# Kernel optimization log

Measured on AMD Instinct MI355X. Metric: run time of the kernel, lower is better.

The kernel has to match this reference:

```python
import jax, jax.numpy as jnp
import numpy as np

H = 768          # hidden_size
V = 32000        # vocab_size
NUM_GATES = 5    # none/dontcare/ptr/yes/no
PAD = 0          # pad_token_id


def setup_inputs() -> dict:
    key = jax.random.key(0)
    ks = jax.random.split(key, 10)
    B, S, J, Ls = 16, 512, 30, 4
    max_len = 8
    sc = 1.0 / np.sqrt(H).astype(np.float32)
    E = jax.random.normal(ks[0], (V, H), jnp.float32) * sc
    E = E.at[PAD].set(0.0)  # padding_idx row is zero
    return dict(
        input_ids=jax.random.randint(ks[1], (B, S), 0, V),
        encoder_output=jax.random.normal(ks[2], (B, S, H), jnp.float32),
        hidden=jax.random.normal(ks[3], (1, B, H), jnp.float32),
        input_masks=jnp.ones((B, S), jnp.int32),  # 1 = valid token
        slot=jax.random.randint(ks[4], (J, Ls), 0, V),
        max_len=max_len,
        E=E,
        W_ih=jax.random.normal(ks[5], (3 * H, H), jnp.float32) * sc,
        W_hh=jax.random.normal(ks[6], (3 * H, H), jnp.float32) * sc,
        b_ih=jnp.zeros((3 * H,), jnp.float32),
        b_hh=jnp.zeros((3 * H,), jnp.float32),
        W_gen=jax.random.normal(ks[7], (3 * H, 1), jnp.float32) * sc,
        b_gen=jnp.zeros((1,), jnp.float32),
        W_gate=jax.random.normal(ks[8], (H, NUM_GATES), jnp.float32) * sc,
        b_gate=jnp.zeros((NUM_GATES,), jnp.float32),
    )


def gru_step(x, h, W_ih, W_hh, b_ih, b_hh):
    # PyTorch GRUCell math
    gi = x @ W_ih.T + b_ih
    gh = h @ W_hh.T + b_hh
    ir, iz, inn = jnp.split(gi, 3, axis=-1)
    hr, hz, hn = jnp.split(gh, 3, axis=-1)
    r = jax.nn.sigmoid(ir + hr)
    z = jax.nn.sigmoid(iz + hz)
    n = jnp.tanh(inn + r * hn)
    return (1.0 - z) * n + z * h


def reference(input_ids, encoder_output, hidden, input_masks, slot, max_len,
              E, W_ih, W_hh, b_ih, b_hh, W_gen, b_gen, W_gate, b_gate):
    B, S, Hd = encoder_output.shape
    J = slot.shape[0]
    mask = input_masks != 1                         # True -> masked (pad)
    slot_e = E[slot].sum(axis=1)                    # [J, H]
    BJ = B * J
    # parallel decoding: flat index = b*J + j (matches repeat/repeat_interleave)
    w = jnp.tile(slot_e, (B, 1))                    # [BJ, H]
    h = jnp.repeat(hidden[0], J, axis=0)            # [BJ, H]
    enc = jnp.repeat(encoder_output, J, axis=0)     # [BJ, S, H]
    ids = jnp.repeat(input_ids, J, axis=0)          # [BJ, S]
    msk = jnp.repeat(mask, J, axis=0)               # [BJ, S]
    rows = jnp.arange(BJ)

    def step(carry, _):
        w, h = carry
        h = gru_step(w, h, W_ih, W_hh, b_ih, b_hh)                    # [BJ, H]
        attn_e = jnp.einsum('bsh,bh->bs', enc, h)                     # [BJ, S]
        attn_e = jnp.where(msk, -1e9, attn_e)
        attn_history = jax.nn.softmax(attn_e, axis=-1)                # [BJ, S]
        attn_vocab = jax.nn.softmax(h @ E.T, axis=-1)                 # [BJ, V]
        context = jnp.einsum('bs,bsh->bh', attn_history, enc)         # [BJ, H]
        p_gen = jax.nn.sigmoid(
            jnp.concatenate([w, h, context], -1) @ W_gen + b_gen)     # [BJ, 1]
        ptr = jnp.zeros_like(attn_vocab).at[rows[:, None], ids].add(attn_history)
        p_final = p_gen * attn_vocab + (1.0 - p_gen) * ptr            # [BJ, V]
        w_next = E[jnp.argmax(p_final, axis=-1)]                      # greedy (teacher=None)
        return (w_next, h), (p_final, context)

    (_, _), (points, contexts) = jax.lax.scan(step, (w, h), None, length=max_len)
    gate_logit = contexts[0] @ W_gate + b_gate                        # gate from step k==0
    all_points = points.transpose(1, 0, 2).reshape(B, J, max_len, V)
    all_gates = gate_logit.reshape(B, J, NUM_GATES)
    return all_points, all_gates
```

## Files before the change

### kernel.cpp

```cpp
#include <hip/hip_runtime.h>
#include <cstdint>
#include <cstddef>

#define HDIM 768
#define VOCAB 32000
#define NGATES 5
#define NJ 30
#define NB 16
#define NS 512
#define NBJ (NB*NJ)
#define G3 2304
#define PR 608
#define NBV 250

typedef _Float16 f16;
typedef _Float16 f16x8 __attribute__((ext_vector_type(8)));
typedef float f32x4 __attribute__((ext_vector_type(4)));

#define GLOBAL_AS __attribute__((address_space(1)))
#define LDS_AS    __attribute__((address_space(3)))

__global__ void k_cast(const float* __restrict__ src, f16* __restrict__ dst, int n) {
    for (int i = blockIdx.x*256 + threadIdx.x; i < n; i += gridDim.x*256)
        dst[i] = (f16)src[i];
}

__global__ void k_cast_split(const float* __restrict__ src, f16* __restrict__ hi,
                             f16* __restrict__ lo, int n) {
    for (int i = blockIdx.x*256 + threadIdx.x; i < n; i += gridDim.x*256) {
        float v = src[i];
        f16 h = (f16)v;
        hi[i] = h;
        lo[i] = (f16)(v - (float)h);
    }
}

__global__ void k_tsplit(const float* __restrict__ enc,
                         f16* __restrict__ encH, f16* __restrict__ encL,
                         f16* __restrict__ encTH, f16* __restrict__ encTL) {
    __shared__ float tile[32][33];
    const int b = blockIdx.x, s0 = blockIdx.y*32, h0 = blockIdx.z*32;
    const int t = threadIdx.x;
    const int hl = t & 31, sl = t >> 5;
    #pragma unroll
    for (int r = 0; r < 4; ++r) {
        int ss = sl + r*8;
        float v = enc[((long)b*NS + s0 + ss)*HDIM + h0 + hl];
        tile[ss][hl] = v;
        f16 h = (f16)v;
        long o = ((long)b*NS + s0 + ss)*HDIM + h0 + hl;
        encH[o] = h; encL[o] = (f16)(v - (float)h);
    }
    __syncthreads();
    #pragma unroll
    for (int r = 0; r < 4; ++r) {
        int hh = sl + r*8;
        float v = tile[hl][hh];
        f16 h = (f16)v;
        long o = ((long)b*HDIM + h0 + hh)*NS + s0 + hl;
        encTH[o] = h; encTL[o] = (f16)(v - (float)h);
    }
}

__global__ void k_init_state(const float* __restrict__ E, const int* __restrict__ slot,
                             const float* __restrict__ hidden,
                             f16* __restrict__ w_hi, f16* __restrict__ w_lo,
                             float* __restrict__ h,
                             f16* __restrict__ h_hi, f16* __restrict__ h_lo) {
    int total = NBJ*HDIM;
    for (int i = blockIdx.x*256 + threadIdx.x; i < total; i += gridDim.x*256) {
        int hh = i % HDIM, row = i / HDIM;
        int b = row / NJ, j = row % NJ;
        float s = 0.f;
        #pragma unroll
        for (int l = 0; l < 4; ++l) s += E[(long)slot[j*4+l]*HDIM + hh];
        f16 sh = (f16)s;
        w_hi[i] = sh; w_lo[i] = (f16)(s - (float)sh);
        float hv = hidden[b*HDIM + hh];
        h[i] = hv;
        f16 hh16 = (f16)hv;
        h_hi[i] = hh16; h_lo[i] = (f16)(hv - (float)hh16);
    }
}

__launch_bounds__(256)
__global__ void k_gemm(const f16* __restrict__ Ah, const f16* __restrict__ Al,
                       const f16* __restrict__ Bh, const f16* __restrict__ Bl,
                       float* __restrict__ Cp, float* __restrict__ psum,
                       int M, long ldc, long coff, int kdim, int nspan,
                       long aBS, long bBS, long cBS) {
    __shared__ f16 a_lds[8][128][8];
    __shared__ f16 b_lds[8][128][8];
    __shared__ float sbuf[2][128];

    const int tid = threadIdx.x;
    const int z = blockIdx.z;
    const int m0 = blockIdx.x*128, n0 = blockIdx.y*128;
    const int w = tid >> 6, lane = tid & 63;
    const int wm = (w >> 1)*64, wn = (w & 1)*64;
    const int lr = lane & 15, lg = lane >> 4;

    f32x4 acc[4][4] = {};

    for (int sp = 0; sp < nspan; ++sp) {
        const f16* Ap = ((sp < 2) ? Ah : Al) + (long)z*aBS;
        const f16* Bp = ((sp == 1) ? Bl : Bh) + (long)z*bBS;
        for (int kc = 0; kc < kdim; kc += 64) {
            #pragma unroll
            for (int i = 0; i < 4; ++i) {
                const int idx = w*4 + i;
                const int c = idx >> 1;
                const int rl = (idx & 1)*64 + lane;
                const f16* ga = Ap + (long)(m0 + rl)*kdim + kc + c*8;
                const f16* gb = Bp + (long)(n0 + rl)*kdim + kc + c*8;
                __builtin_amdgcn_global_load_lds(
                    (const GLOBAL_AS unsigned int*)ga,
                    (LDS_AS unsigned int*)((char*)&a_lds[0][0][0] + idx*1024), 16, 0, 0);
                __builtin_amdgcn_global_load_lds(
                    (const GLOBAL_AS unsigned int*)gb,
                    (LDS_AS unsigned int*)((char*)&b_lds[0][0][0] + idx*1024), 16, 0, 0);
            }
            __syncthreads();
            #pragma unroll
            for (int kk = 0; kk < 2; ++kk) {
                const int c = kk*4 + lg;
                f16x8 af[4], bf[4];
                #pragma unroll
                for (int mi = 0; mi < 4; ++mi) af[mi] = *(const f16x8*)&a_lds[c][wm + mi*16 + lr][0];
                #pragma unroll
                for (int nf = 0; nf < 4; ++nf) bf[nf] = *(const f16x8*)&b_lds[c][wn + nf*16 + lr][0];
                #pragma unroll
                for (int mi = 0; mi < 4; ++mi)
                    #pragma unroll
                    for (int nf = 0; nf < 4; ++nf)
                        acc[mi][nf] = __builtin_amdgcn_mfma_f32_16x16x32_f16(af[mi], bf[nf], acc[mi][nf], 0, 0, 0);
            }
            __syncthreads();
        }
    }

    float* Cb = Cp + (long)z*cBS + coff;
    #pragma unroll
    for (int mi = 0; mi < 4; ++mi) {
        #pragma unroll
        for (int nf = 0; nf < 4; ++nf) {
            int col = n0 + wn + nf*16 + lr;
            int rowb = m0 + wm + mi*16 + lg*4;
            #pragma unroll
            for (int r = 0; r < 4; ++r) {
                int row = rowb + r;
                if (row < M) Cb[(long)row*ldc + col] = acc[mi][nf][r];
            }
        }
    }

    if (psum != nullptr) {
        #pragma unroll
        for (int mi = 0; mi < 4; ++mi) {
            #pragma unroll
            for (int r = 0; r < 4; ++r) {
                float s = 0.f;
                #pragma unroll
                for (int nf = 0; nf < 4; ++nf) s += expf(acc[mi][nf][r]);
                s += __shfl_xor(s, 1); s += __shfl_xor(s, 2);
                s += __shfl_xor(s, 4); s += __shfl_xor(s, 8);
                if (lr == 0) sbuf[w & 1][wm + mi*16 + lg*4 + r] = s;
            }
        }
        __syncthreads();
        if (tid < 128)
            psum[(long)blockIdx.y*512 + m0 + tid] = sbuf[0][tid] + sbuf[1][tid];
    }
}

__global__ void k_gru_elem(const float* __restrict__ gi, const float* __restrict__ gh,
                           const float* __restrict__ bih, const float* __restrict__ bhh,
                           float* __restrict__ h, f16* __restrict__ h_hi, f16* __restrict__ h_lo) {
    int total = NBJ*HDIM;
    for (int i = blockIdx.x*256 + threadIdx.x; i < total; i += gridDim.x*256) {
        int c = i % HDIM; long row = i / HDIM;
        long base = row*G3;
        float r = gi[base + c]        + bih[c]        + gh[base + c]        + bhh[c];
        float z = gi[base + 768 + c]  + bih[768 + c]  + gh[base + 768 + c]  + bhh[768 + c];
        float hn = gh[base + 1536 + c] + bhh[1536 + c];
        float in_ = gi[base + 1536 + c] + bih[1536 + c];
        r = 1.f/(1.f + expf(-r));
        z = 1.f/(1.f + expf(-z));
        float n = tanhf(in_ + r*hn);
        float hv = (1.f - z)*n + z*h[i];
        h[i] = hv;
        f16 hh16 = (f16)hv;
        h_hi[i] = hh16; h_lo[i] = (f16)(hv - (float)hh16);
    }
}

__launch_bounds__(256)
__global__ void k_softmax_s(float* __restrict__ ae, const int* __restrict__ masks,
                            f16* __restrict__ ahH, f16* __restrict__ ahL) {
    const int row = blockIdx.x, tid = threadIdx.x;
    const int b = row / NJ;
    __shared__ float red[256];
    float x0 = ae[(long)row*NS + tid];
    float x1 = ae[(long)row*NS + tid + 256];
    if (masks[b*NS + tid]       != 1) x0 = -1e9f;
    if (masks[b*NS + tid + 256] != 1) x1 = -1e9f;
    red[tid] = fmaxf(x0, x1); __syncthreads();
    for (int o = 128; o > 0; o >>= 1) { if (tid < o) red[tid] = fmaxf(red[tid], red[tid+o]); __syncthreads(); }
    float m = red[0]; __syncthreads();
    float e0 = expf(x0 - m), e1 = expf(x1 - m);
    red[tid] = e0 + e1; __syncthreads();
    for (int o = 128; o > 0; o >>= 1) { if (tid < o) red[tid] += red[tid+o]; __syncthreads(); }
    float inv = 1.f/red[0];
    float p0 = e0*inv, p1 = e1*inv;
    ae[(long)row*NS + tid]       = p0;
    ae[(long)row*NS + tid + 256] = p1;
    f16 a0 = (f16)p0, a1 = (f16)p1;
    ahH[(long)row*NS + tid]       = a0; ahL[(long)row*NS + tid]       = (f16)(p0 - (float)a0);
    ahH[(long)row*NS + tid + 256] = a1; ahL[(long)row*NS + tid + 256] = (f16)(p1 - (float)a1);
}

__launch_bounds__(64)
__global__ void k_pgen(const f16* __restrict__ w_hi, const f16* __restrict__ w_lo,
                       const float* __restrict__ h,
                       const float* __restrict__ ctx, const float* __restrict__ Wgen,
                       const float* __restrict__ bgen, const float* __restrict__ Wgate,
                       const float* __restrict__ bgate, float* __restrict__ pgen,
                       float* __restrict__ out_gates, int do_gate) {
    const int row = blockIdx.x, lane = threadIdx.x;
    float acc = 0.f;
    for (int x = lane; x < HDIM; x += 64) {
        float wv = (float)w_hi[(long)row*HDIM + x] + (float)w_lo[(long)row*HDIM + x];
        acc += wv                          * Wgen[x];
        acc += h[(long)row*HDIM + x]       * Wgen[768 + x];
        acc += ctx[(long)row*HDIM + x]     * Wgen[1536 + x];
    }
    for (int o = 32; o > 0; o >>= 1) acc += __shfl_down(acc, o);
    if (lane == 0) pgen[row] = 1.f/(1.f + expf(-(acc + bgen[0])));
    if (do_gate) {
        for (int g = 0; g < NGATES; ++g) {
            float a = 0.f;
            for (int x = lane; x < HDIM; x += 64) a += ctx[(long)row*HDIM + x]*Wgate[x*NGATES + g];
            for (int o = 32; o > 0; o >>= 1) a += __shfl_down(a, o);
            if (lane == 0) out_gates[row*NGATES + g] = a + bgate[g];
        }
    }
}

__launch_bounds__(256)
__global__ void k_finalize(float* __restrict__ pts, long ldrow, long coff,
                           const float* __restrict__ psum, const float* __restrict__ pgen,
                           const int* __restrict__ ids, const float* __restrict__ ah,
                           const float* __restrict__ E,
                           f16* __restrict__ w_hi, f16* __restrict__ w_lo) {
    const int row = blockIdx.x, tid = threadIdx.x;
    const int b = row / NJ;
    float* base = pts + (long)row*ldrow + coff;

    __shared__ float red[256];
    float s = 0.f;
    for (int nb = tid; nb < NBV; nb += 256) s += psum[(long)nb*512 + row];
    red[tid] = s; __syncthreads();
    for (int o = 128; o > 0; o >>= 1) { if (tid < o) red[tid] += red[tid+o]; __syncthreads(); }
    const float pg = pgen[row];
    const float scale = pg / red[0];

    float bv = -1.f; int bi = 0;
    for (int v = tid; v < VOCAB; v += 256) {
        float val = scale*expf(base[v]);
        base[v] = val;
        if (val > bv) { bv = val; bi = v; }
    }
    __shared__ float rv[256]; __shared__ int ri[256];
    rv[tid] = bv; ri[tid] = bi; __syncthreads();
    for (int o = 128; o > 0; o >>= 1) {
        if (tid < o) {
            float v2 = rv[tid+o]; int i2 = ri[tid+o];
            if (v2 > rv[tid] || (v2 == rv[tid] && i2 < ri[tid])) { rv[tid] = v2; ri[tid] = i2; }
        }
        __syncthreads();
    }
    float v0 = rv[0]; int i0 = ri[0];
    __syncthreads();

    const float cp = 1.f - pg;
    float sv = -1.f; int si = 0x7FFFFFFF;
    for (int ss = tid; ss < NS; ss += 256) {
        int id = ids[(long)b*NS + ss];
        float add = cp * ah[(long)row*NS + ss];
        float old = atomicAdd(base + id, add);
        float cand = old + add;
        if (cand > sv || (cand == sv && id < si)) { sv = cand; si = id; }
    }
    rv[tid] = sv; ri[tid] = si; __syncthreads();
    for (int o = 128; o > 0; o >>= 1) {
        if (tid < o) {
            float v2 = rv[tid+o]; int i2 = ri[tid+o];
            if (v2 > rv[tid] || (v2 == rv[tid] && i2 < ri[tid])) { rv[tid] = v2; ri[tid] = i2; }
        }
        __syncthreads();
    }
    __shared__ int bidx;
    if (tid == 0) {
        int ii = i0; float vv = v0;
        if (rv[0] > vv || (rv[0] == vv && ri[0] < ii)) { vv = rv[0]; ii = ri[0]; }
        bidx = ii;
    }
    __syncthreads();
    const int idx = bidx;
    for (int x = tid; x < HDIM; x += 256) {
        float ev = E[(long)idx*HDIM + x];
        f16 eh = (f16)ev;
        w_hi[(long)row*HDIM + x] = eh;
        w_lo[(long)row*HDIM + x] = (f16)(ev - (float)eh);
    }
}

extern "C" void kernel_launch(void* const* d_in, const int* in_sizes, int n_in,
                              void* d_out, int out_size, void* d_ws, size_t ws_size,
                              hipStream_t stream) {
    const int*   input_ids = (const int*)  d_in[0];
    const float* enc       = (const float*)d_in[1];
    const float* hidden    = (const float*)d_in[2];
    const int*   masks     = (const int*)  d_in[3];
    const int*   slot      = (const int*)  d_in[4];
    const float* E     = (const float*)d_in[6];
    const float* Wih   = (const float*)d_in[7];
    const float* Whh   = (const float*)d_in[8];
    const float* bih   = (const float*)d_in[9];
    const float* bhh   = (const float*)d_in[10];
    const float* Wgen  = (const float*)d_in[11];
    const float* bgen  = (const float*)d_in[12];
    const float* Wgate = (const float*)d_in[13];
    const float* bgate = (const float*)d_in[14];

    const int ml = (out_size / NBJ - NGATES) / VOCAB;
    float* out = (float*)d_out;
    float* gates_out = out + (long)NBJ*ml*VOCAB;

    char* ws = (char*)d_ws;
    auto carve = [&](size_t bytes) { char* p = ws; ws += (bytes + 255) & ~(size_t)255; return p; };
    f16*   E16   = (f16*)carve((size_t)VOCAB*HDIM*2);
    f16*   WH2   = (f16*)carve((size_t)2*G3*HDIM*2);
    f16*   WL2   = (f16*)carve((size_t)2*G3*HDIM*2);
    f16*   SH    = (f16*)carve((size_t)2*PR*HDIM*2);
    f16*   SL    = (f16*)carve((size_t)2*PR*HDIM*2);
    float* gigh  = (float*)carve((size_t)2*NBJ*G3*4);
    f16*   encH  = (f16*)carve((size_t)NB*NS*HDIM*2);
    f16*   encL  = (f16*)carve((size_t)NB*NS*HDIM*2);
    f16*   encTH = (f16*)carve((size_t)NB*HDIM*NS*2);
    f16*   encTL = (f16*)carve((size_t)NB*HDIM*NS*2);
    float* hbuf  = (float*)carve((size_t)NBJ*HDIM*4);
    float* ae    = (float*)carve((size_t)NBJ*NS*4);
    f16*   ahH   = (f16*)carve((size_t)PR*NS*2);
    f16*   ahL   = (f16*)carve((size_t)PR*NS*2);
    float* ctx   = (float*)carve((size_t)NBJ*HDIM*4);
    float* pgen  = (float*)carve((size_t)NBJ*4);
    float* ps    = (float*)carve((size_t)NBV*512*4);

    f16* WihH = WH2;  f16* WihL = WL2;
    f16* wH = SH;     f16* wL = SL;
    f16* hH = SH + (size_t)PR*HDIM;
    f16* hL = SL + (size_t)PR*HDIM;
    float* gi = gigh; float* gh = gigh + (size_t)NBJ*G3;

    k_cast<<<8192, 256, 0, stream>>>(E, E16, VOCAB*HDIM);
    k_cast_split<<<2048, 256, 0, stream>>>(Wih, WihH, WihL, G3*HDIM);
    k_cast_split<<<2048, 256, 0, stream>>>(Whh, WH2 + (size_t)G3*HDIM, WL2 + (size_t)G3*HDIM, G3*HDIM);
    k_tsplit<<<dim3(NB, 16, 24), 256, 0, stream>>>(enc, encH, encL, encTH, encTL);
    k_init_state<<<1440, 256, 0, stream>>>(E, slot, hidden, wH, wL, hbuf, hH, hL);

    const long ldrow = (long)ml*VOCAB;
    for (int t = 0; t < ml; ++t) {
        k_gemm<<<dim3(4, 18, 2), 256, 0, stream>>>(wH, wL, WihH, WihL, gigh, nullptr,
            NBJ, (long)G3, 0, HDIM, 3, (long)PR*HDIM, (long)G3*HDIM, (long)NBJ*G3);
        k_gru_elem<<<1440, 256, 0, stream>>>(gi, gh, bih, bhh, hbuf, hH, hL);
        k_gemm<<<dim3(1, 4, NB), 256, 0, stream>>>(hH, hL, encH, encL, ae, nullptr,
            NJ, (long)NS, 0, HDIM, 3, (long)NJ*HDIM, (long)NS*HDIM, (long)NJ*NS);
        k_softmax_s<<<NBJ, 256, 0, stream>>>(ae, masks, ahH, ahL);
        k_gemm<<<dim3(1, 6, NB), 256, 0, stream>>>(ahH, ahL, encTH, encTL, ctx, nullptr,
            NJ, (long)HDIM, 0, NS, 3, (long)NJ*NS, (long)HDIM*NS, (long)NJ*HDIM);
        k_pgen<<<NBJ, 64, 0, stream>>>(wH, wL, hbuf, ctx, Wgen, bgen, Wgate, bgate,
                                       pgen, gates_out, t == 0 ? 1 : 0);
        k_gemm<<<dim3(4, NBV, 1), 256, 0, stream>>>(hH, hL, E16, nullptr, out, ps,
            NBJ, ldrow, (long)t*VOCAB, HDIM, 1, 0, 0, 0);
        k_finalize<<<NBJ, 256, 0, stream>>>(out, ldrow, (long)t*VOCAB, ps, pgen,
                                            input_ids, ae, E, wH, wL);
    }
}
```

Measured before the change: 2.768 ms.

## Replace split-fp16 attention GEMMs with fp32 kernels and split vocab finalize

```diff
diff --git a/kernel.cpp b/kernel.cpp
--- a/kernel.cpp
+++ b/kernel.cpp
@@ -35,33 +35,6 @@
     }
 }
 
-__global__ void k_tsplit(const float* __restrict__ enc,
-                         f16* __restrict__ encH, f16* __restrict__ encL,
-                         f16* __restrict__ encTH, f16* __restrict__ encTL) {
-    __shared__ float tile[32][33];
-    const int b = blockIdx.x, s0 = blockIdx.y*32, h0 = blockIdx.z*32;
-    const int t = threadIdx.x;
-    const int hl = t & 31, sl = t >> 5;
-    #pragma unroll
-    for (int r = 0; r < 4; ++r) {
-        int ss = sl + r*8;
-        float v = enc[((long)b*NS + s0 + ss)*HDIM + h0 + hl];
-        tile[ss][hl] = v;
-        f16 h = (f16)v;
-        long o = ((long)b*NS + s0 + ss)*HDIM + h0 + hl;
-        encH[o] = h; encL[o] = (f16)(v - (float)h);
-    }
-    __syncthreads();
-    #pragma unroll
-    for (int r = 0; r < 4; ++r) {
-        int hh = sl + r*8;
-        float v = tile[hl][hh];
-        f16 h = (f16)v;
-        long o = ((long)b*HDIM + h0 + hh)*NS + s0 + hl;
-        encTH[o] = h; encTL[o] = (f16)(v - (float)h);
-    }
-}
-
 __global__ void k_init_state(const float* __restrict__ E, const int* __restrict__ slot,
                              const float* __restrict__ hidden,
                              f16* __restrict__ w_hi, f16* __restrict__ w_lo,
@@ -86,7 +59,8 @@
 __launch_bounds__(256)
 __global__ void k_gemm(const f16* __restrict__ Ah, const f16* __restrict__ Al,
                        const f16* __restrict__ Bh, const f16* __restrict__ Bl,
-                       float* __restrict__ Cp, float* __restrict__ psum,
+                       float* __restrict__ Cf, f16* __restrict__ Ch,
+                       float* __restrict__ psum,
                        int M, long ldc, long coff, int kdim, int nspan,
                        long aBS, long bBS, long cBS) {
     __shared__ f16 a_lds[8][128][8];
@@ -139,19 +113,34 @@
         }
     }
 
-    float* Cb = Cp + (long)z*cBS + coff;
-    #pragma unroll
-    for (int mi = 0; mi < 4; ++mi) {
-        #pragma unroll
-        for (int nf = 0; nf < 4; ++nf) {
-            int col = n0 + wn + nf*16 + lr;
-            int rowb = m0 + wm + mi*16 + lg*4;
-            #pragma unroll
-            for (int r = 0; r < 4; ++r) {
-                int row = rowb + r;
-                if (row < M) Cb[(long)row*ldc + col] = acc[mi][nf][r];
-            }
-        }
+    if (Ch != nullptr) {
+        f16* Cb = Ch + (long)z*cBS + coff;
+        #pragma unroll
+        for (int mi = 0; mi < 4; ++mi)
+            #pragma unroll
+            for (int nf = 0; nf < 4; ++nf) {
+                int col = n0 + wn + nf*16 + lr;
+                int rowb = m0 + wm + mi*16 + lg*4;
+                #pragma unroll
+                for (int r = 0; r < 4; ++r) {
+                    int row = rowb + r;
+                    if (row < M) Cb[(long)row*ldc + col] = (f16)acc[mi][nf][r];
+                }
+            }
+    } else {
+        float* Cb = Cf + (long)z*cBS + coff;
+        #pragma unroll
+        for (int mi = 0; mi < 4; ++mi)
+            #pragma unroll
+            for (int nf = 0; nf < 4; ++nf) {
+                int col = n0 + wn + nf*16 + lr;
+                int rowb = m0 + wm + mi*16 + lg*4;
+                #pragma unroll
+                for (int r = 0; r < 4; ++r) {
+                    int row = rowb + r;
+                    if (row < M) Cb[(long)row*ldc + col] = acc[mi][nf][r];
+                }
+            }
     }
 
     if (psum != nullptr) {
@@ -161,7 +150,7 @@
             for (int r = 0; r < 4; ++r) {
                 float s = 0.f;
                 #pragma unroll
-                for (int nf = 0; nf < 4; ++nf) s += expf(acc[mi][nf][r]);
+                for (int nf = 0; nf < 4; ++nf) s += expf((float)(f16)acc[mi][nf][r]);
                 s += __shfl_xor(s, 1); s += __shfl_xor(s, 2);
                 s += __shfl_xor(s, 4); s += __shfl_xor(s, 8);
                 if (lr == 0) sbuf[w & 1][wm + mi*16 + lg*4 + r] = s;
@@ -195,11 +184,60 @@
 }
 
 __launch_bounds__(256)
-__global__ void k_softmax_s(float* __restrict__ ae, const int* __restrict__ masks,
-                            f16* __restrict__ ahH, f16* __restrict__ ahL) {
+__global__ void k_attn(const float* __restrict__ h, const float* __restrict__ enc,
+                       float* __restrict__ attn_e) {
+    __shared__ float h_lds[NJ][64];
+    __shared__ float e_lds[64][65];
+    const int b = blockIdx.x, st = blockIdx.y;
+    const int s0 = st*64;
+    const int tid = threadIdx.x;
+    const int s = tid & 63, jg = tid >> 6;
+    float acc[8] = {};
+    for (int kc = 0; kc < HDIM; kc += 64) {
+        for (int idx = tid; idx < NJ*64; idx += 256) {
+            int j = idx >> 6, k = idx & 63;
+            h_lds[j][k] = h[((long)(b*NJ + j))*HDIM + kc + k];
+        }
+        #pragma unroll
+        for (int i = 0; i < 4; ++i) {
+            int id = tid + i*256;
+            int ss = id >> 4, kq = (id & 15)*4;
+            float4 v = *(const float4*)&enc[((long)b*NS + s0 + ss)*HDIM + kc + kq];
+            e_lds[ss][kq+0] = v.x; e_lds[ss][kq+1] = v.y;
+            e_lds[ss][kq+2] = v.z; e_lds[ss][kq+3] = v.w;
+        }
+        __syncthreads();
+        for (int k = 0; k < 64; ++k) {
+            float e = e_lds[s][k];
+            #pragma unroll
+            for (int i = 0; i < 8; ++i) {
+                int j = jg + i*4;
+                if (j < NJ) acc[i] += h_lds[j][k]*e;
+            }
+        }
+        __syncthreads();
+    }
+    #pragma unroll
+    for (int i = 0; i < 8; ++i) {
+        int j = jg + i*4;
+        if (j < NJ) attn_e[((long)(b*NJ + j))*NS + s0 + s] = acc[i];
+    }
+}
+
+__launch_bounds__(256)
+__global__ void k_smctxpg(float* __restrict__ ae, const int* __restrict__ masks,
+                          const float* __restrict__ enc,
+                          const f16* __restrict__ w_hi, const f16* __restrict__ w_lo,
+                          const float* __restrict__ h,
+                          const float* __restrict__ Wgen, const float* __restrict__ bgen,
+                          const float* __restrict__ Wgate, const float* __restrict__ bgate,
+                          float* __restrict__ pgen, float* __restrict__ out_gates, int do_gate) {
     const int row = blockIdx.x, tid = threadIdx.x;
     const int b = row / NJ;
     __shared__ float red[256];
+    __shared__ float ah_l[NS];
+    __shared__ float ctx_l[HDIM];
+
     float x0 = ae[(long)row*NS + tid];
     float x1 = ae[(long)row*NS + tid + 256];
     if (masks[b*NS + tid]       != 1) x0 = -1e9f;
@@ -214,60 +252,60 @@
     float p0 = e0*inv, p1 = e1*inv;
     ae[(long)row*NS + tid]       = p0;
     ae[(long)row*NS + tid + 256] = p1;
-    f16 a0 = (f16)p0, a1 = (f16)p1;
-    ahH[(long)row*NS + tid]       = a0; ahL[(long)row*NS + tid]       = (f16)(p0 - (float)a0);
-    ahH[(long)row*NS + tid + 256] = a1; ahL[(long)row*NS + tid + 256] = (f16)(p1 - (float)a1);
-}
-
-__launch_bounds__(64)
-__global__ void k_pgen(const f16* __restrict__ w_hi, const f16* __restrict__ w_lo,
-                       const float* __restrict__ h,
-                       const float* __restrict__ ctx, const float* __restrict__ Wgen,
-                       const float* __restrict__ bgen, const float* __restrict__ Wgate,
-                       const float* __restrict__ bgate, float* __restrict__ pgen,
-                       float* __restrict__ out_gates, int do_gate) {
-    const int row = blockIdx.x, lane = threadIdx.x;
+    ah_l[tid] = p0; ah_l[tid + 256] = p1;
+    __syncthreads();
+
+    const float* eb = enc + (long)b*NS*HDIM;
+    float c0 = 0.f, c1 = 0.f, c2 = 0.f;
+    for (int s = 0; s < NS; ++s) {
+        float a = ah_l[s];
+        const float* er = eb + (long)s*HDIM;
+        c0 += a*er[tid]; c1 += a*er[tid + 256]; c2 += a*er[tid + 512];
+    }
+    ctx_l[tid] = c0; ctx_l[tid + 256] = c1; ctx_l[tid + 512] = c2;
+    __syncthreads();
+
     float acc = 0.f;
-    for (int x = lane; x < HDIM; x += 64) {
+    for (int x = tid; x < HDIM; x += 256) {
         float wv = (float)w_hi[(long)row*HDIM + x] + (float)w_lo[(long)row*HDIM + x];
-        acc += wv                          * Wgen[x];
-        acc += h[(long)row*HDIM + x]       * Wgen[768 + x];
-        acc += ctx[(long)row*HDIM + x]     * Wgen[1536 + x];
-    }
-    for (int o = 32; o > 0; o >>= 1) acc += __shfl_down(acc, o);
-    if (lane == 0) pgen[row] = 1.f/(1.f + expf(-(acc + bgen[0])));
+        acc += wv*Wgen[x] + h[(long)row*HDIM + x]*Wgen[768 + x] + ctx_l[x]*Wgen[1536 + x];
+    }
+    red[tid] = acc; __syncthreads();
+    for (int o = 128; o > 0; o >>= 1) { if (tid < o) red[tid] += red[tid+o]; __syncthreads(); }
+    if (tid == 0) pgen[row] = 1.f/(1.f + expf(-(red[0] + bgen[0])));
+
     if (do_gate) {
         for (int g = 0; g < NGATES; ++g) {
+            __syncthreads();
             float a = 0.f;
-            for (int x = lane; x < HDIM; x += 64) a += ctx[(long)row*HDIM + x]*Wgate[x*NGATES + g];
-            for (int o = 32; o > 0; o >>= 1) a += __shfl_down(a, o);
-            if (lane == 0) out_gates[row*NGATES + g] = a + bgate[g];
+            for (int x = tid; x < HDIM; x += 256) a += ctx_l[x]*Wgate[x*NGATES + g];
+            red[tid] = a; __syncthreads();
+            for (int o = 128; o > 0; o >>= 1) { if (tid < o) red[tid] += red[tid+o]; __syncthreads(); }
+            if (tid == 0) out_gates[row*NGATES + g] = red[0] + bgate[g];
         }
     }
 }
 
 __launch_bounds__(256)
-__global__ void k_finalize(float* __restrict__ pts, long ldrow, long coff,
-                           const float* __restrict__ psum, const float* __restrict__ pgen,
-                           const int* __restrict__ ids, const float* __restrict__ ah,
-                           const float* __restrict__ E,
-                           f16* __restrict__ w_hi, f16* __restrict__ w_lo) {
-    const int row = blockIdx.x, tid = threadIdx.x;
-    const int b = row / NJ;
-    float* base = pts + (long)row*ldrow + coff;
-
+__global__ void k_scale(const f16* __restrict__ l16, float* __restrict__ out,
+                        long ldrow, long coff,
+                        const float* __restrict__ psum, const float* __restrict__ pgen,
+                        unsigned long long* __restrict__ pamax) {
+    const int row = blockIdx.x, c = blockIdx.y, tid = threadIdx.x;
     __shared__ float red[256];
     float s = 0.f;
     for (int nb = tid; nb < NBV; nb += 256) s += psum[(long)nb*512 + row];
     red[tid] = s; __syncthreads();
     for (int o = 128; o > 0; o >>= 1) { if (tid < o) red[tid] += red[tid+o]; __syncthreads(); }
-    const float pg = pgen[row];
-    const float scale = pg / red[0];
-
-    float bv = -1.f; int bi = 0;
-    for (int v = tid; v < VOCAB; v += 256) {
-        float val = scale*expf(base[v]);
-        base[v] = val;
+    const float scale = pgen[row] / red[0];
+
+    const f16* lb = l16 + (long)row*VOCAB;
+    float* ob = out + (long)row*ldrow + coff;
+    const int v0 = c*4000;
+    float bv = -1.f; int bi = 0x7FFFFFFF;
+    for (int v = v0 + tid; v < v0 + 4000; v += 256) {
+        float val = scale*expf((float)lb[v]);
+        ob[v] = val;
         if (val > bv) { bv = val; bi = v; }
     }
     __shared__ float rv[256]; __shared__ int ri[256];
@@ -279,10 +317,22 @@
         }
         __syncthreads();
     }
-    float v0 = rv[0]; int i0 = ri[0];
-    __syncthreads();
-
-    const float cp = 1.f - pg;
+    if (tid == 0)
+        pamax[(long)row*8 + c] = ((unsigned long long)__float_as_uint(rv[0]) << 32)
+                               | (unsigned long long)(0xFFFFFFFFu - (unsigned)ri[0]);
+}
+
+__launch_bounds__(256)
+__global__ void k_scatter(float* __restrict__ pts, long ldrow, long coff,
+                          const int* __restrict__ ids, const float* __restrict__ ah,
+                          const float* __restrict__ pgen,
+                          const unsigned long long* __restrict__ pamax,
+                          const float* __restrict__ E,
+                          f16* __restrict__ w_hi, f16* __restrict__ w_lo) {
+    const int row = blockIdx.x, tid = threadIdx.x;
+    const int b = row / NJ;
+    float* base = pts + (long)row*ldrow + coff;
+    const float cp = 1.f - pgen[row];
     float sv = -1.f; int si = 0x7FFFFFFF;
     for (int ss = tid; ss < NS; ss += 256) {
         int id = ids[(long)b*NS + ss];
@@ -291,6 +341,7 @@
         float cand = old + add;
         if (cand > sv || (cand == sv && id < si)) { sv = cand; si = id; }
     }
+    __shared__ float rv[256]; __shared__ int ri[256];
     rv[tid] = sv; ri[tid] = si; __syncthreads();
     for (int o = 128; o > 0; o >>= 1) {
         if (tid < o) {
@@ -301,8 +352,14 @@
     }
     __shared__ int bidx;
     if (tid == 0) {
-        int ii = i0; float vv = v0;
-        if (rv[0] > vv || (rv[0] == vv && ri[0] < ii)) { vv = rv[0]; ii = ri[0]; }
+        float vv = rv[0]; int ii = ri[0];
+        #pragma unroll
+        for (int cc = 0; cc < 8; ++cc) {
+            unsigned long long pk = pamax[(long)row*8 + cc];
+            float pv = __uint_as_float((unsigned)(pk >> 32));
+            int pi = (int)(0xFFFFFFFFu - (unsigned)(pk & 0xFFFFFFFFu));
+            if (pv > vv || (pv == vv && pi < ii)) { vv = pv; ii = pi; }
+        }
         bidx = ii;
     }
     __syncthreads();
@@ -345,45 +402,38 @@
     f16*   SH    = (f16*)carve((size_t)2*PR*HDIM*2);
     f16*   SL    = (f16*)carve((size_t)2*PR*HDIM*2);
     float* gigh  = (float*)carve((size_t)2*NBJ*G3*4);
-    f16*   encH  = (f16*)carve((size_t)NB*NS*HDIM*2);
-    f16*   encL  = (f16*)carve((size_t)NB*NS*HDIM*2);
-    f16*   encTH = (f16*)carve((size_t)NB*HDIM*NS*2);
-    f16*   encTL = (f16*)carve((size_t)NB*HDIM*NS*2);
     float* hbuf  = (float*)carve((size_t)NBJ*HDIM*4);
     float* ae    = (float*)carve((size_t)NBJ*NS*4);
-    f16*   ahH   = (f16*)carve((size_t)PR*NS*2);
-    f16*   ahL   = (f16*)carve((size_t)PR*NS*2);
-    float* ctx   = (float*)carve((size_t)NBJ*HDIM*4);
+    f16*   l16   = (f16*)carve((size_t)NBJ*VOCAB*2);
     float* pgen  = (float*)carve((size_t)NBJ*4);
     float* ps    = (float*)carve((size_t)NBV*512*4);
+    unsigned long long* pamax = (unsigned long long*)carve((size_t)NBJ*8*8);
 
     f16* WihH = WH2;  f16* WihL = WL2;
     f16* wH = SH;     f16* wL = SL;
     f16* hH = SH + (size_t)PR*HDIM;
     f16* hL = SL + (size_t)PR*HDIM;
     float* gi = gigh; float* gh = gigh + (size_t)NBJ*G3;
+    (void)gi; (void)gh;
 
     k_cast<<<8192, 256, 0, stream>>>(E, E16, VOCAB*HDIM);
     k_cast_split<<<2048, 256, 0, stream>>>(Wih, WihH, WihL, G3*HDIM);
     k_cast_split<<<2048, 256, 0, stream>>>(Whh, WH2 + (size_t)G3*HDIM, WL2 + (size_t)G3*HDIM, G3*HDIM);
-    k_tsplit<<<dim3(NB, 16, 24), 256, 0, stream>>>(enc, encH, encL, encTH, encTL);
     k_init_state<<<1440, 256, 0, stream>>>(E, slot, hidden, wH, wL, hbuf, hH, hL);
 
     const long ldrow = (long)ml*VOCAB;
     for (int t = 0; t < ml; ++t) {
-        k_gemm<<<dim3(4, 18, 2), 256, 0, stream>>>(wH, wL, WihH, WihL, gigh, nullptr,
+        k_gemm<<<dim3(4, 18, 2), 256, 0, stream>>>(wH, wL, WihH, WihL, gigh, nullptr, nullptr,
             NBJ, (long)G3, 0, HDIM, 3, (long)PR*HDIM, (long)G3*HDIM, (long)NBJ*G3);
-        k_gru_elem<<<1440, 256, 0, stream>>>(gi, gh, bih, bhh, hbuf, hH, hL);
-        k_gemm<<<dim3(1, 4, NB), 256, 0, stream>>>(hH, hL, encH, encL, ae, nullptr,
-            NJ, (long)NS, 0, HDIM, 3, (long)NJ*HDIM, (long)NS*HDIM, (long)NJ*NS);
-        k_softmax_s<<<NBJ, 256, 0, stream>>>(ae, masks, ahH, ahL);
-        k_gemm<<<dim3(1, 6, NB), 256, 0, stream>>>(ahH, ahL, encTH, encTL, ctx, nullptr,
-            NJ, (long)HDIM, 0, NS, 3, (long)NJ*NS, (long)HDIM*NS, (long)NJ*HDIM);
-        k_pgen<<<NBJ, 64, 0, stream>>>(wH, wL, hbuf, ctx, Wgen, bgen, Wgate, bgate,
-                                       pgen, gates_out, t == 0 ? 1 : 0);
-        k_gemm<<<dim3(4, NBV, 1), 256, 0, stream>>>(hH, hL, E16, nullptr, out, ps,
-            NBJ, ldrow, (long)t*VOCAB, HDIM, 1, 0, 0, 0);
-        k_finalize<<<NBJ, 256, 0, stream>>>(out, ldrow, (long)t*VOCAB, ps, pgen,
-                                            input_ids, ae, E, wH, wL);
-    }
-}
+        k_gru_elem<<<1440, 256, 0, stream>>>(gigh, gigh + (size_t)NBJ*G3, bih, bhh, hbuf, hH, hL);
+        k_attn<<<dim3(NB, 8), 256, 0, stream>>>(hbuf, enc, ae);
+        k_smctxpg<<<NBJ, 256, 0, stream>>>(ae, masks, enc, wH, wL, hbuf,
+                                           Wgen, bgen, Wgate, bgate,
+                                           pgen, gates_out, t == 0 ? 1 : 0);
+        k_gemm<<<dim3(4, NBV, 1), 256, 0, stream>>>(hH, hL, E16, nullptr, nullptr, l16, ps,
+            NBJ, (long)VOCAB, 0, HDIM, 1, 0, 0, 0);
+        k_scale<<<dim3(NBJ, 8), 256, 0, stream>>>(l16, out, ldrow, (long)t*VOCAB, ps, pgen, pamax);
+        k_scatter<<<NBJ, 256, 0, stream>>>(out, ldrow, (long)t*VOCAB, input_ids, ae, pgen,
+                                           pamax, E, wH, wL);
+    }
+}
```

Measured after the change: 3.223 ms. 16.4% more time.
